# Kernel optimization log

Measured on AMD Instinct MI355X. Metric: run time of the kernel, lower is better.

Reference implementation:

```python
import jax, jax.numpy as jnp
import numpy as np

N_NODES = 50000
N_EDGES = 800000
IN_C = 256
HID_C = 256
OUT_C = 128
N_GRAPHS = 256


def setup_inputs() -> dict:
    key = jax.random.key(0)
    ks = jax.random.split(key, 12)
    x = jax.random.normal(ks[0], (N_NODES, IN_C), dtype=jnp.float32)
    src = jax.random.randint(ks[1], (N_EDGES,), 0, N_NODES, dtype=jnp.int32)
    dst = jnp.sort(jax.random.randint(ks[2], (N_EDGES,), 0, N_NODES, dtype=jnp.int32))
    p = jax.random.uniform(ks[3], (N_NODES,), dtype=jnp.float32)
    batch = jnp.sort(jax.random.randint(ks[4], (N_NODES,), 0, N_GRAPHS, dtype=jnp.int32))
    root_ptr = jax.random.randint(ks[5], (N_GRAPHS,), 0, N_NODES, dtype=jnp.int32)
    s1 = 1.0 / np.sqrt(IN_C)
    s2 = 1.0 / np.sqrt(HID_C)
    s3 = 1.0 / np.sqrt(2 * HID_C)
    Wl1 = jax.random.uniform(ks[6], (IN_C, HID_C), jnp.float32, -s1, s1)
    Wr1 = jax.random.uniform(ks[7], (IN_C, HID_C), jnp.float32, -s1, s1)
    b1 = jnp.zeros((HID_C,), jnp.float32)
    Wl2 = jax.random.uniform(ks[8], (HID_C, HID_C), jnp.float32, -s2, s2)
    Wr2 = jax.random.uniform(ks[9], (HID_C, HID_C), jnp.float32, -s2, s2)
    b2 = jnp.zeros((HID_C,), jnp.float32)
    Wlin = jax.random.uniform(ks[10], (2 * HID_C, OUT_C), jnp.float32, -s3, s3)
    blin = jax.random.uniform(ks[11], (OUT_C,), jnp.float32, -s3, s3)
    return {"x": x, "src": src, "dst": dst, "p": p, "batch": batch,
            "root_ptr": root_ptr, "num_graphs": N_GRAPHS,
            "Wl1": Wl1, "Wr1": Wr1, "b1": b1,
            "Wl2": Wl2, "Wr2": Wr2, "b2": b2,
            "Wlin": Wlin, "blin": blin}


def _sage_conv(x, src, dst, inv_deg, Wl, Wr, b):
    # mean aggregation of neighbor features: scatter-add then divide by degree
    agg = jax.ops.segment_sum(x[src], dst, num_segments=N_NODES)  # [N, d]
    agg = agg * inv_deg[:, None]
    return agg @ Wl + x @ Wr + b


def reference(x, src, dst, p, batch, root_ptr, num_graphs,
              Wl1, Wr1, b1, Wl2, Wr2, b2, Wlin, blin):
    # in-degree for mean aggregation (shared by both convs)
    deg = jax.ops.segment_sum(jnp.ones_like(dst, dtype=x.dtype), dst,
                              num_segments=N_NODES)
    inv_deg = jnp.where(deg > 0, 1.0 / jnp.maximum(deg, 1.0), 0.0)

    h = _sage_conv(x, src, dst, inv_deg, Wl1, Wr1, b1)
    h = jax.nn.relu(h)  # dropout is identity in eval mode
    h = _sage_conv(h, src, dst, inv_deg, Wl2, Wr2, b2)

    # masked mean pool of p-weighted features per graph
    pw = h * p[:, None]
    gsum = jax.ops.segment_sum(pw, batch, num_segments=num_graphs)
    gcnt = jax.ops.segment_sum(jnp.ones_like(p), batch, num_segments=num_graphs)
    gmean = gsum / jnp.maximum(gcnt, 1.0)[:, None]

    feat = jnp.concatenate([h[root_ptr], gmean], axis=-1)  # [G, 2*hid]
    return feat @ Wlin + blin
```

## Files before the change

kernel.cpp:

```cpp
#include <hip/hip_runtime.h>
#include <hip/hip_bf16.h>

#define N_NODES 50000
#define N_EDGES 800000
#define C_DIM   256
#define OUT_C   128
#define N_GRAPHS 256

typedef unsigned short ushort8 __attribute__((ext_vector_type(8)));
typedef __bf16         bf16x8  __attribute__((ext_vector_type(8)));
typedef float          f32x4   __attribute__((ext_vector_type(4)));

typedef __attribute__((address_space(1))) const unsigned int gu32;
typedef __attribute__((address_space(3))) unsigned int lu32;

#if __has_builtin(__builtin_amdgcn_sched_barrier)
#define SCHED_FENCE() __builtin_amdgcn_sched_barrier(0)
#else
#define SCHED_FENCE() ((void)0)
#endif

__device__ __forceinline__ float us2f(unsigned short u) {
    unsigned int x = ((unsigned int)u) << 16;
    return __builtin_bit_cast(float, x);
}
__device__ __forceinline__ unsigned short f2bf(float f) {
    unsigned int u = __builtin_bit_cast(unsigned int, f);
    u += 0x7fffu + ((u >> 16) & 1u);
    return (unsigned short)(u >> 16);
}

__device__ __forceinline__ int lower_bound_i(const int* __restrict__ a, int n, int v) {
    int lo = 0, hi = n;
    while (lo < hi) {
        int mid = (lo + hi) >> 1;
        if (a[mid] < v) lo = mid + 1; else hi = mid;
    }
    return lo;
}

__global__ void preprocess(const float* __restrict__ x, unsigned short* __restrict__ xb,
                           const float* __restrict__ W0, const float* __restrict__ W1,
                           const float* __restrict__ W2, const float* __restrict__ W3,
                           unsigned short* __restrict__ D0, unsigned short* __restrict__ D1,
                           unsigned short* __restrict__ D2, unsigned short* __restrict__ D3,
                           const int* __restrict__ dst, const int* __restrict__ batch,
                           int* __restrict__ row_ptr, int* __restrict__ graph_ptr,
                           float* __restrict__ inv_deg) {
    int b = blockIdx.x;
    int t = threadIdx.x;
    if (b < 12500) {
        int i = b * 256 + t;
        float4 v = *(const float4*)(x + ((size_t)i << 2));
        ushort4 o;
        o.x = f2bf(v.x); o.y = f2bf(v.y); o.z = f2bf(v.z); o.w = f2bf(v.w);
        *(ushort4*)(xb + ((size_t)i << 2)) = o;
    } else if (b < 13524) {
        int sub = b - 12500;
        const float* S; unsigned short* D;
        switch (sub >> 8) {
            case 0: S = W0; D = D0; break;
            case 1: S = W1; D = D1; break;
            case 2: S = W2; D = D2; break;
            default: S = W3; D = D3; break;
        }
        int i = (sub & 255) * 256 + t;
        int k = i >> 8, n = i & 255;
        D[n * 256 + k] = f2bf(S[i]);
    } else {
        int i = (b - 13524) * 256 + t;
        if (i <= N_NODES) {
            int lb = lower_bound_i(dst, N_EDGES, i);
            row_ptr[i] = lb;
            if (i < N_NODES) {
                int ub = lower_bound_i(dst, N_EDGES, i + 1);
                int cnt = ub - lb;
                inv_deg[i] = (cnt > 0) ? (1.0f / (float)cnt) : 0.0f;
            }
        }
        if (i <= N_GRAPHS) graph_ptr[i] = lower_bound_i(batch, N_NODES, i);
    }
}

__global__ void aggregate(const unsigned short* __restrict__ X,
                          const int* __restrict__ src,
                          const int* __restrict__ row_ptr,
                          const float* __restrict__ inv_deg,
                          unsigned short* __restrict__ out) {
    int gw   = (blockIdx.x * blockDim.x + threadIdx.x) >> 6;
    int lane = threadIdx.x & 63;
    if (gw >= N_NODES) return;
    int e0 = row_ptr[gw], e1 = row_ptr[gw + 1];
    const int lo = lane << 2;
    float a0 = 0.f, a1 = 0.f, a2 = 0.f, a3 = 0.f;
    int e = e0;

    for (; e + 16 <= e1; e += 16) {
        ushort4 v[16];
#pragma unroll
        for (int j = 0; j < 16; ++j) {
            int s = __builtin_amdgcn_readfirstlane(src[e + j]);
            v[j] = *(const ushort4*)(X + ((size_t)s << 8) + lo);
        }
        SCHED_FENCE();
#pragma unroll
        for (int j = 0; j < 16; ++j) {
            a0 += us2f(v[j].x); a1 += us2f(v[j].y);
            a2 += us2f(v[j].z); a3 += us2f(v[j].w);
        }
    }
    int rem = e1 - e;
    if (rem > 0) {
        int cl = e1 - 1;
        ushort4 v[16]; float w[16];
#pragma unroll
        for (int j = 0; j < 16; ++j) {
            int ej = e + j;
            int ec = ej < cl ? ej : cl;
            w[j] = (ej < e1) ? 1.0f : 0.0f;
            int s = __builtin_amdgcn_readfirstlane(src[ec]);
            v[j] = *(const ushort4*)(X + ((size_t)s << 8) + lo);
        }
        SCHED_FENCE();
#pragma unroll
        for (int j = 0; j < 16; ++j) {
            a0 = fmaf(us2f(v[j].x), w[j], a0);
            a1 = fmaf(us2f(v[j].y), w[j], a1);
            a2 = fmaf(us2f(v[j].z), w[j], a2);
            a3 = fmaf(us2f(v[j].w), w[j], a3);
        }
    }

    float sc = inv_deg[gw];
    ushort4 o;
    o.x = f2bf(a0 * sc); o.y = f2bf(a1 * sc); o.z = f2bf(a2 * sc); o.w = f2bf(a3 * sc);
    *(ushort4*)(out + ((size_t)gw << 8) + lo) = o;
}

__global__ __launch_bounds__(512, 2)
void gemm_fused(const unsigned short* __restrict__ A1,
                const unsigned short* __restrict__ A2,
                const unsigned short* __restrict__ B1t,
                const unsigned short* __restrict__ B2t,
                const float* __restrict__ bias,
                unsigned short* __restrict__ C,
                int M, int do_relu) {
    __shared__ __align__(16) unsigned short As[8192];
    __shared__ __align__(16) unsigned short Bs[16384];

    const int t    = threadIdx.x;
    const int m0   = blockIdx.x * 128;
    const int lane = t & 63, wid = t >> 6;
    const int wm   = (wid >> 2) * 64;
    const int wn   = (wid & 3) * 64;
    const int lrow = lane & 15;
    const int kq   = lane >> 4;

    const f32x4 zero4 = {0.f, 0.f, 0.f, 0.f};
    f32x4 acc[4][4];
#pragma unroll
    for (int i = 0; i < 4; ++i)
#pragma unroll
        for (int j = 0; j < 4; ++j) acc[i][j] = zero4;

    for (int it = 0; it < 8; ++it) {
        const unsigned short* __restrict__ Ab = (it < 4) ? A1 : A2;
        const unsigned short* __restrict__ Bb = (it < 4) ? B1t : B2t;
        int ko = (it * 64) & 255;

#pragma unroll
        for (int i = 0; i < 2; ++i) {
            int q   = t + i * 512;
            int row = q >> 3;
            int kb  = (q & 7) ^ (row & 7);
            const unsigned short* ga = Ab + (size_t)(m0 + row) * 256 + ko + kb * 8;
            __builtin_amdgcn_global_load_lds((gu32*)ga, (lu32*)(As + q * 8), 16, 0, 0);
        }
#pragma unroll
        for (int i = 0; i < 4; ++i) {
            int q   = t + i * 512;
            int row = q >> 3;
            int kb  = (q & 7) ^ (row & 7);
            const unsigned short* gb = Bb + (size_t)row * 256 + ko + kb * 8;
            __builtin_amdgcn_global_load_lds((gu32*)gb, (lu32*)(Bs + q * 8), 16, 0, 0);
        }
        __syncthreads();

#pragma unroll
        for (int s = 0; s < 2; ++s) {
            int kqp = s * 4 + kq;
            bf16x8 af[4], bfr[4];
#pragma unroll
            for (int mi = 0; mi < 4; ++mi) {
                int r = wm + mi * 16 + lrow;
                int slot = r * 8 + (kqp ^ (lrow & 7));
                uint4 u = *(const uint4*)(As + slot * 8);
                af[mi] = __builtin_bit_cast(bf16x8, u);
            }
#pragma unroll
            for (int ni = 0; ni < 4; ++ni) {
                int r = wn + ni * 16 + lrow;
                int slot = r * 8 + (kqp ^ (lrow & 7));
                uint4 u = *(const uint4*)(Bs + slot * 8);
                bfr[ni] = __builtin_bit_cast(bf16x8, u);
            }
#pragma unroll
            for (int mi = 0; mi < 4; ++mi)
#pragma unroll
                for (int ni = 0; ni < 4; ++ni)
                    acc[mi][ni] = __builtin_amdgcn_mfma_f32_16x16x32_bf16(
                        af[mi], bfr[ni], acc[mi][ni], 0, 0, 0);
        }
        __syncthreads();
    }

    const int rbase = (lane >> 4) * 4;
#pragma unroll
    for (int ni = 0; ni < 4; ++ni) {
        int n  = wn + ni * 16 + lrow;
        float bv = bias[n];
#pragma unroll
        for (int mi = 0; mi < 4; ++mi) {
            int mb = m0 + wm + mi * 16 + rbase;
#pragma unroll
            for (int r = 0; r < 4; ++r) {
                int m = mb + r;
                if (m < M) {
                    float v = acc[mi][ni][r] + bv;
                    if (do_relu) v = fmaxf(v, 0.f);
                    C[(size_t)m * 256 + n] = f2bf(v);
                }
            }
        }
    }
}

__global__ void pool_final(const unsigned short* __restrict__ h2,
                           const float* __restrict__ p,
                           const int* __restrict__ graph_ptr,
                           const int* __restrict__ root_ptr,
                           const float* __restrict__ Wlin,
                           const float* __restrict__ blin,
                           float* __restrict__ out) {
    __shared__ float fl[512];
    int g = blockIdx.x;
    int c = threadIdx.x;
    int s = graph_ptr[g], e = graph_ptr[g + 1];
    float acc = 0.f;
    for (int n = s; n < e; n += 8) {
        int cl = e - 1;
        float w[8]; unsigned short v[8];
#pragma unroll
        for (int j = 0; j < 8; ++j) {
            int nj = n + j;
            int ncj = nj < cl ? nj : cl;
            int nu = __builtin_amdgcn_readfirstlane(ncj);
            w[j] = (nj < e) ? p[nu] : 0.0f;
            v[j] = h2[(size_t)nu * 256 + c];
        }
        SCHED_FENCE();
#pragma unroll
        for (int j = 0; j < 8; ++j)
            acc = fmaf(us2f(v[j]), w[j], acc);
    }
    float cnt = (float)(e - s);
    int root = root_ptr[g];
    fl[c]       = us2f(h2[(size_t)root * 256 + c]);
    fl[256 + c] = acc / fmaxf(cnt, 1.0f);
    __syncthreads();

    int o = threadIdx.x;
    if (o < 128) {
        float s0 = 0.f, s1 = 0.f, s2 = 0.f, s3 = 0.f;
        for (int k = 0; k < 512; k += 4) {
            s0 = fmaf(fl[k + 0], Wlin[(k + 0) * 128 + o], s0);
            s1 = fmaf(fl[k + 1], Wlin[(k + 1) * 128 + o], s1);
            s2 = fmaf(fl[k + 2], Wlin[(k + 2) * 128 + o], s2);
            s3 = fmaf(fl[k + 3], Wlin[(k + 3) * 128 + o], s3);
        }
        out[(size_t)g * 128 + o] = blin[o] + ((s0 + s1) + (s2 + s3));
    }
}

extern "C" void kernel_launch(void* const* d_in, const int* in_sizes, int n_in,
                              void* d_out, int out_size, void* d_ws, size_t ws_size,
                              hipStream_t stream) {
    const float* x        = (const float*)d_in[0];
    const int*   src      = (const int*)d_in[1];
    const int*   dst      = (const int*)d_in[2];
    const float* p        = (const float*)d_in[3];
    const int*   batch    = (const int*)d_in[4];
    const int*   root_ptr = (const int*)d_in[5];
    const float* Wl1  = (const float*)d_in[7];
    const float* Wr1  = (const float*)d_in[8];
    const float* b1   = (const float*)d_in[9];
    const float* Wl2  = (const float*)d_in[10];
    const float* Wr2  = (const float*)d_in[11];
    const float* b2   = (const float*)d_in[12];
    const float* Wlin = (const float*)d_in[13];
    const float* blin = (const float*)d_in[14];
    float* out = (float*)d_out;

    size_t off = 0;
    char* base = (char*)d_ws;
    auto alloc = [&](size_t bytes) -> void* {
        void* q = base + off;
        off += (bytes + 255) & ~(size_t)255;
        return q;
    };
    int*            row_ptr   = (int*)  alloc((N_NODES + 1) * sizeof(int));
    int*            graph_ptr = (int*)  alloc((N_GRAPHS + 1) * sizeof(int));
    float*          inv_deg   = (float*)alloc(N_NODES * sizeof(float));
    unsigned short* Wl1t = (unsigned short*)alloc(256 * 256 * 2);
    unsigned short* Wr1t = (unsigned short*)alloc(256 * 256 * 2);
    unsigned short* Wl2t = (unsigned short*)alloc(256 * 256 * 2);
    unsigned short* Wr2t = (unsigned short*)alloc(256 * 256 * 2);
    unsigned short* xb   = (unsigned short*)alloc((size_t)N_NODES * 256 * 2);
    unsigned short* aggb = (unsigned short*)alloc((size_t)N_NODES * 256 * 2);
    unsigned short* h1   = (unsigned short*)alloc((size_t)N_NODES * 256 * 2);
    unsigned short* h2   = (unsigned short*)alloc((size_t)N_NODES * 256 * 2);
    (void)ws_size; (void)n_in; (void)in_sizes; (void)out_size;

    preprocess<<<13720, 256, 0, stream>>>(x, xb, Wl1, Wr1, Wl2, Wr2,
                                          Wl1t, Wr1t, Wl2t, Wr2t,
                                          dst, batch, row_ptr, graph_ptr, inv_deg);

    dim3 ggrid((N_NODES + 127) / 128);

    aggregate<<<N_NODES / 4, 256, 0, stream>>>(xb, src, row_ptr, inv_deg, aggb);
    gemm_fused<<<ggrid, 512, 0, stream>>>(aggb, xb, Wl1t, Wr1t, b1, h1, N_NODES, 1);

    aggregate<<<N_NODES / 4, 256, 0, stream>>>(h1, src, row_ptr, inv_deg, aggb);
    gemm_fused<<<ggrid, 512, 0, stream>>>(aggb, h1, Wl2t, Wr2t, b2, h2, N_NODES, 0);

    pool_final<<<N_GRAPHS, 256, 0, stream>>>(h2, p, graph_ptr, root_ptr,
                                             Wlin, blin, out);
}
```

Baseline: 316.8 us.

## Load GEMM MFMA operands directly from global memory instead of LDS tiles

The fused SAGE GEMM no longer stages A and B tiles through shared memory with global_load_lds and barriers. Each wave now reads its bf16x8 MFMA fragments straight from global memory and relies on L1/L2 caching for reuse. The kernel's launch-bounds occupancy hint is raised from 2 to 4, since no LDS is used and the per-iteration syncthreads are gone. In exchange, each B and A fragment is fetched redundantly by several waves, which adds global and cache traffic and exposes load latency.

```diff
diff --git a/kernel.cpp b/kernel.cpp
--- a/kernel.cpp
+++ b/kernel.cpp
@@ -10,9 +10,6 @@
 typedef unsigned short ushort8 __attribute__((ext_vector_type(8)));
 typedef __bf16         bf16x8  __attribute__((ext_vector_type(8)));
 typedef float          f32x4   __attribute__((ext_vector_type(4)));
-
-typedef __attribute__((address_space(1))) const unsigned int gu32;
-typedef __attribute__((address_space(3))) unsigned int lu32;
 
 #if __has_builtin(__builtin_amdgcn_sched_barrier)
 #define SCHED_FENCE() __builtin_amdgcn_sched_barrier(0)
@@ -137,17 +134,14 @@
     *(ushort4*)(out + ((size_t)gw << 8) + lo) = o;
 }
 
-__global__ __launch_bounds__(512, 2)
-void gemm_fused(const unsigned short* __restrict__ A1,
-                const unsigned short* __restrict__ A2,
-                const unsigned short* __restrict__ B1t,
-                const unsigned short* __restrict__ B2t,
-                const float* __restrict__ bias,
-                unsigned short* __restrict__ C,
-                int M, int do_relu) {
-    __shared__ __align__(16) unsigned short As[8192];
-    __shared__ __align__(16) unsigned short Bs[16384];
-
+__global__ __launch_bounds__(512, 4)
+void gemm_direct(const unsigned short* __restrict__ A1,
+                 const unsigned short* __restrict__ A2,
+                 const unsigned short* __restrict__ B1t,
+                 const unsigned short* __restrict__ B2t,
+                 const float* __restrict__ bias,
+                 unsigned short* __restrict__ C,
+                 int M, int do_relu) {
     const int t    = threadIdx.x;
     const int m0   = blockIdx.x * 128;
     const int lane = t & 63, wid = t >> 6;
@@ -163,45 +157,26 @@
 #pragma unroll
         for (int j = 0; j < 4; ++j) acc[i][j] = zero4;
 
+    const size_t arow = (size_t)(m0 + wm + lrow) * 256;
+    const size_t brow = (size_t)(wn + lrow) * 256;
+
     for (int it = 0; it < 8; ++it) {
         const unsigned short* __restrict__ Ab = (it < 4) ? A1 : A2;
         const unsigned short* __restrict__ Bb = (it < 4) ? B1t : B2t;
         int ko = (it * 64) & 255;
 
 #pragma unroll
-        for (int i = 0; i < 2; ++i) {
-            int q   = t + i * 512;
-            int row = q >> 3;
-            int kb  = (q & 7) ^ (row & 7);
-            const unsigned short* ga = Ab + (size_t)(m0 + row) * 256 + ko + kb * 8;
-            __builtin_amdgcn_global_load_lds((gu32*)ga, (lu32*)(As + q * 8), 16, 0, 0);
-        }
-#pragma unroll
-        for (int i = 0; i < 4; ++i) {
-            int q   = t + i * 512;
-            int row = q >> 3;
-            int kb  = (q & 7) ^ (row & 7);
-            const unsigned short* gb = Bb + (size_t)row * 256 + ko + kb * 8;
-            __builtin_amdgcn_global_load_lds((gu32*)gb, (lu32*)(Bs + q * 8), 16, 0, 0);
-        }
-        __syncthreads();
-
-#pragma unroll
         for (int s = 0; s < 2; ++s) {
-            int kqp = s * 4 + kq;
+            int kk = ko + s * 32 + kq * 8;
             bf16x8 af[4], bfr[4];
 #pragma unroll
             for (int mi = 0; mi < 4; ++mi) {
-                int r = wm + mi * 16 + lrow;
-                int slot = r * 8 + (kqp ^ (lrow & 7));
-                uint4 u = *(const uint4*)(As + slot * 8);
+                uint4 u = *(const uint4*)(Ab + arow + (size_t)mi * 16 * 256 + kk);
                 af[mi] = __builtin_bit_cast(bf16x8, u);
             }
 #pragma unroll
             for (int ni = 0; ni < 4; ++ni) {
-                int r = wn + ni * 16 + lrow;
-                int slot = r * 8 + (kqp ^ (lrow & 7));
-                uint4 u = *(const uint4*)(Bs + slot * 8);
+                uint4 u = *(const uint4*)(Bb + brow + (size_t)ni * 16 * 256 + kk);
                 bfr[ni] = __builtin_bit_cast(bf16x8, u);
             }
 #pragma unroll
@@ -211,7 +186,6 @@
                     acc[mi][ni] = __builtin_amdgcn_mfma_f32_16x16x32_bf16(
                         af[mi], bfr[ni], acc[mi][ni], 0, 0, 0);
         }
-        __syncthreads();
     }
 
     const int rbase = (lane >> 4) * 4;
@@ -328,10 +302,10 @@
     dim3 ggrid((N_NODES + 127) / 128);
 
     aggregate<<<N_NODES / 4, 256, 0, stream>>>(xb, src, row_ptr, inv_deg, aggb);
-    gemm_fused<<<ggrid, 512, 0, stream>>>(aggb, xb, Wl1t, Wr1t, b1, h1, N_NODES, 1);
+    gemm_direct<<<ggrid, 512, 0, stream>>>(aggb, xb, Wl1t, Wr1t, b1, h1, N_NODES, 1);
 
     aggregate<<<N_NODES / 4, 256, 0, stream>>>(h1, src, row_ptr, inv_deg, aggb);
-    gemm_fused<<<ggrid, 512, 0, stream>>>(aggb, h1, Wl2t, Wr2t, b2, h2, N_NODES, 0);
+    gemm_direct<<<ggrid, 512, 0, stream>>>(aggb, h1, Wl2t, Wr2t, b2, h2, N_NODES, 0);
 
     pool_final<<<N_GRAPHS, 256, 0, stream>>>(h2, p, graph_ptr, root_ptr,
                                              Wlin, blin, out);
```

New measurement: 402.5 us. 27.1% more time.

## Overlap root-weight GEMM with neighbor aggregation in one heterogeneous launch

Applied to the files above, without the earlier changes.

Splits each SAGE layer's GEMM into two halves. The x@Wr half runs in the same kernel launch as the neighbor gather-aggregation, using separate block ranges, so tensor-core work can overlap the memory-bound gather. The finish kernel then computes only agg@Wl and adds the stored bf16 partial plus the bias. This adds a bf16 round-trip of the partial product through global memory, with an extra rounding step. It also adds a second GEMM tiling for the partial, whose LDS layout is unswizzled and may cause bank conflicts.

```diff
diff --git a/kernel.cpp b/kernel.cpp
--- a/kernel.cpp
+++ b/kernel.cpp
@@ -82,69 +82,142 @@
     }
 }
 
-__global__ void aggregate(const unsigned short* __restrict__ X,
-                          const int* __restrict__ src,
-                          const int* __restrict__ row_ptr,
-                          const float* __restrict__ inv_deg,
-                          unsigned short* __restrict__ out) {
-    int gw   = (blockIdx.x * blockDim.x + threadIdx.x) >> 6;
-    int lane = threadIdx.x & 63;
-    if (gw >= N_NODES) return;
-    int e0 = row_ptr[gw], e1 = row_ptr[gw + 1];
-    const int lo = lane << 2;
-    float a0 = 0.f, a1 = 0.f, a2 = 0.f, a3 = 0.f;
-    int e = e0;
-
-    for (; e + 16 <= e1; e += 16) {
-        ushort4 v[16];
-#pragma unroll
-        for (int j = 0; j < 16; ++j) {
-            int s = __builtin_amdgcn_readfirstlane(src[e + j]);
-            v[j] = *(const ushort4*)(X + ((size_t)s << 8) + lo);
-        }
-        SCHED_FENCE();
-#pragma unroll
-        for (int j = 0; j < 16; ++j) {
-            a0 += us2f(v[j].x); a1 += us2f(v[j].y);
-            a2 += us2f(v[j].z); a3 += us2f(v[j].w);
-        }
-    }
-    int rem = e1 - e;
-    if (rem > 0) {
-        int cl = e1 - 1;
-        ushort4 v[16]; float w[16];
-#pragma unroll
-        for (int j = 0; j < 16; ++j) {
-            int ej = e + j;
-            int ec = ej < cl ? ej : cl;
-            w[j] = (ej < e1) ? 1.0f : 0.0f;
-            int s = __builtin_amdgcn_readfirstlane(src[ec]);
-            v[j] = *(const ushort4*)(X + ((size_t)s << 8) + lo);
-        }
-        SCHED_FENCE();
-#pragma unroll
-        for (int j = 0; j < 16; ++j) {
-            a0 = fmaf(us2f(v[j].x), w[j], a0);
-            a1 = fmaf(us2f(v[j].y), w[j], a1);
-            a2 = fmaf(us2f(v[j].z), w[j], a2);
-            a3 = fmaf(us2f(v[j].w), w[j], a3);
-        }
-    }
-
-    float sc = inv_deg[gw];
-    ushort4 o;
-    o.x = f2bf(a0 * sc); o.y = f2bf(a1 * sc); o.z = f2bf(a2 * sc); o.w = f2bf(a3 * sc);
-    *(ushort4*)(out + ((size_t)gw << 8) + lo) = o;
+__global__ void hetero(const unsigned short* __restrict__ X,
+                       const int* __restrict__ src,
+                       const int* __restrict__ row_ptr,
+                       const float* __restrict__ inv_deg,
+                       unsigned short* __restrict__ aggb,
+                       const unsigned short* __restrict__ Brt,
+                       unsigned short* __restrict__ Cpart) {
+    __shared__ __align__(16) unsigned short As[4096];
+    __shared__ __align__(16) unsigned short Bs[4096];
+
+    const int b = blockIdx.x;
+    const int t = threadIdx.x;
+
+    if (b < 782) {
+        const int m0   = (b >> 1) * 128;
+        const int n0   = (b & 1) * 128;
+        const int lane = t & 63, wid = t >> 6;
+        const int wm   = (wid >> 1) * 64;
+        const int wn   = (wid & 1) * 64;
+        const int lrow = lane & 15;
+        const int kq   = lane >> 4;
+
+        const f32x4 zero4 = {0.f, 0.f, 0.f, 0.f};
+        f32x4 acc[4][4];
+#pragma unroll
+        for (int i = 0; i < 4; ++i)
+#pragma unroll
+            for (int j = 0; j < 4; ++j) acc[i][j] = zero4;
+
+        for (int it = 0; it < 8; ++it) {
+            int ko = it * 32;
+#pragma unroll
+            for (int i = 0; i < 2; ++i) {
+                int q   = t + i * 256;
+                int row = q & 127;
+                int kb  = q >> 7;
+                const unsigned short* ga = X + (size_t)(m0 + row) * 256 + ko + kb * 8;
+                __builtin_amdgcn_global_load_lds((gu32*)ga, (lu32*)(As + q * 8), 16, 0, 0);
+                const unsigned short* gb = Brt + (size_t)(n0 + row) * 256 + ko + kb * 8;
+                __builtin_amdgcn_global_load_lds((gu32*)gb, (lu32*)(Bs + q * 8), 16, 0, 0);
+            }
+            __syncthreads();
+
+            bf16x8 af[4], bfr[4];
+#pragma unroll
+            for (int mi = 0; mi < 4; ++mi) {
+                uint4 u = *(const uint4*)(As + ((kq * 128) + wm + mi * 16 + lrow) * 8);
+                af[mi] = __builtin_bit_cast(bf16x8, u);
+            }
+#pragma unroll
+            for (int ni = 0; ni < 4; ++ni) {
+                uint4 u = *(const uint4*)(Bs + ((kq * 128) + wn + ni * 16 + lrow) * 8);
+                bfr[ni] = __builtin_bit_cast(bf16x8, u);
+            }
+#pragma unroll
+            for (int mi = 0; mi < 4; ++mi)
+#pragma unroll
+                for (int ni = 0; ni < 4; ++ni)
+                    acc[mi][ni] = __builtin_amdgcn_mfma_f32_16x16x32_bf16(
+                        af[mi], bfr[ni], acc[mi][ni], 0, 0, 0);
+            __syncthreads();
+        }
+
+        const int rbase = (lane >> 4) * 4;
+#pragma unroll
+        for (int ni = 0; ni < 4; ++ni) {
+            int n = n0 + wn + ni * 16 + lrow;
+#pragma unroll
+            for (int mi = 0; mi < 4; ++mi) {
+                int mb = m0 + wm + mi * 16 + rbase;
+#pragma unroll
+                for (int r = 0; r < 4; ++r) {
+                    int m = mb + r;
+                    if (m < N_NODES)
+                        Cpart[(size_t)m * 256 + n] = f2bf(acc[mi][ni][r]);
+                }
+            }
+        }
+    } else {
+        int gw   = (b - 782) * 4 + (t >> 6);
+        int lane = t & 63;
+        if (gw >= N_NODES) return;
+        int e0 = row_ptr[gw], e1 = row_ptr[gw + 1];
+        const int lo = lane << 2;
+        float a0 = 0.f, a1 = 0.f, a2 = 0.f, a3 = 0.f;
+        int e = e0;
+
+        for (; e + 16 <= e1; e += 16) {
+            ushort4 v[16];
+#pragma unroll
+            for (int j = 0; j < 16; ++j) {
+                int s = __builtin_amdgcn_readfirstlane(src[e + j]);
+                v[j] = *(const ushort4*)(X + ((size_t)s << 8) + lo);
+            }
+            SCHED_FENCE();
+#pragma unroll
+            for (int j = 0; j < 16; ++j) {
+                a0 += us2f(v[j].x); a1 += us2f(v[j].y);
+                a2 += us2f(v[j].z); a3 += us2f(v[j].w);
+            }
+        }
+        if (e < e1) {
+            int cl = e1 - 1;
+            ushort4 v[16]; float w[16];
+#pragma unroll
+            for (int j = 0; j < 16; ++j) {
+                int ej = e + j;
+                int ec = ej < cl ? ej : cl;
+                w[j] = (ej < e1) ? 1.0f : 0.0f;
+                int s = __builtin_amdgcn_readfirstlane(src[ec]);
+                v[j] = *(const ushort4*)(X + ((size_t)s << 8) + lo);
+            }
+            SCHED_FENCE();
+#pragma unroll
+            for (int j = 0; j < 16; ++j) {
+                a0 = fmaf(us2f(v[j].x), w[j], a0);
+                a1 = fmaf(us2f(v[j].y), w[j], a1);
+                a2 = fmaf(us2f(v[j].z), w[j], a2);
+                a3 = fmaf(us2f(v[j].w), w[j], a3);
+            }
+        }
+
+        float sc = inv_deg[gw];
+        ushort4 o;
+        o.x = f2bf(a0 * sc); o.y = f2bf(a1 * sc); o.z = f2bf(a2 * sc); o.w = f2bf(a3 * sc);
+        *(ushort4*)(aggb + ((size_t)gw << 8) + lo) = o;
+    }
 }
 
 __global__ __launch_bounds__(512, 2)
-void gemm_fused(const unsigned short* __restrict__ A1,
-                const unsigned short* __restrict__ A2,
-                const unsigned short* __restrict__ B1t,
-                const unsigned short* __restrict__ B2t,
-                const float* __restrict__ bias,
-                unsigned short* __restrict__ C,
-                int M, int do_relu) {
+void finish(const unsigned short* __restrict__ A,
+            const unsigned short* __restrict__ Blt,
+            const unsigned short* __restrict__ Cpart,
+            const float* __restrict__ bias,
+            unsigned short* __restrict__ C,
+            int do_relu) {
     __shared__ __align__(16) unsigned short As[8192];
     __shared__ __align__(16) unsigned short Bs[16384];
 
@@ -163,17 +236,14 @@
 #pragma unroll
         for (int j = 0; j < 4; ++j) acc[i][j] = zero4;
 
-    for (int it = 0; it < 8; ++it) {
-        const unsigned short* __restrict__ Ab = (it < 4) ? A1 : A2;
-        const unsigned short* __restrict__ Bb = (it < 4) ? B1t : B2t;
-        int ko = (it * 64) & 255;
-
+    for (int it = 0; it < 4; ++it) {
+        int ko = it * 64;
 #pragma unroll
         for (int i = 0; i < 2; ++i) {
             int q   = t + i * 512;
             int row = q >> 3;
             int kb  = (q & 7) ^ (row & 7);
-            const unsigned short* ga = Ab + (size_t)(m0 + row) * 256 + ko + kb * 8;
+            const unsigned short* ga = A + (size_t)(m0 + row) * 256 + ko + kb * 8;
             __builtin_amdgcn_global_load_lds((gu32*)ga, (lu32*)(As + q * 8), 16, 0, 0);
         }
 #pragma unroll
@@ -181,7 +251,7 @@
             int q   = t + i * 512;
             int row = q >> 3;
             int kb  = (q & 7) ^ (row & 7);
-            const unsigned short* gb = Bb + (size_t)row * 256 + ko + kb * 8;
+            const unsigned short* gb = Blt + (size_t)row * 256 + ko + kb * 8;
             __builtin_amdgcn_global_load_lds((gu32*)gb, (lu32*)(Bs + q * 8), 16, 0, 0);
         }
         __syncthreads();
@@ -225,8 +295,8 @@
 #pragma unroll
             for (int r = 0; r < 4; ++r) {
                 int m = mb + r;
-                if (m < M) {
-                    float v = acc[mi][ni][r] + bv;
+                if (m < N_NODES) {
+                    float v = acc[mi][ni][r] + bv + us2f(Cpart[(size_t)m * 256 + n]);
                     if (do_relu) v = fmaxf(v, 0.f);
                     C[(size_t)m * 256 + n] = f2bf(v);
                 }
@@ -318,20 +388,19 @@
     unsigned short* xb   = (unsigned short*)alloc((size_t)N_NODES * 256 * 2);
     unsigned short* aggb = (unsigned short*)alloc((size_t)N_NODES * 256 * 2);
     unsigned short* h1   = (unsigned short*)alloc((size_t)N_NODES * 256 * 2);
-    unsigned short* h2   = (unsigned short*)alloc((size_t)N_NODES * 256 * 2);
+    unsigned short* Cpart= (unsigned short*)alloc((size_t)N_NODES * 256 * 2);
+    unsigned short* h2   = xb;
     (void)ws_size; (void)n_in; (void)in_sizes; (void)out_size;
 
     preprocess<<<13720, 256, 0, stream>>>(x, xb, Wl1, Wr1, Wl2, Wr2,
                                           Wl1t, Wr1t, Wl2t, Wr2t,
                                           dst, batch, row_ptr, graph_ptr, inv_deg);
 
-    dim3 ggrid((N_NODES + 127) / 128);
-
-    aggregate<<<N_NODES / 4, 256, 0, stream>>>(xb, src, row_ptr, inv_deg, aggb);
-    gemm_fused<<<ggrid, 512, 0, stream>>>(aggb, xb, Wl1t, Wr1t, b1, h1, N_NODES, 1);
-
-    aggregate<<<N_NODES / 4, 256, 0, stream>>>(h1, src, row_ptr, inv_deg, aggb);
-    gemm_fused<<<ggrid, 512, 0, stream>>>(aggb, h1, Wl2t, Wr2t, b2, h2, N_NODES, 0);
+    hetero<<<13282, 256, 0, stream>>>(xb, src, row_ptr, inv_deg, aggb, Wr1t, Cpart);
+    finish<<<391, 512, 0, stream>>>(aggb, Wl1t, Cpart, b1, h1, 1);
+
+    hetero<<<13282, 256, 0, stream>>>(h1, src, row_ptr, inv_deg, aggb, Wr2t, Cpart);
+    finish<<<391, 512, 0, stream>>>(aggb, Wl2t, Cpart, b2, h2, 0);
 
     pool_final<<<N_GRAPHS, 256, 0, stream>>>(h2, p, graph_ptr, root_ptr,
                                              Wlin, blin, out);
```

New measurement: 380.4 us. 1.2x slower.
